# Optimization experiments

Hardware: AMD Instinct MI355X
Metric: run time of the kernel (lower is better)

The kernel has to match this reference:

```python
import jax, jax.numpy as jnp
import numpy as np

HIDDEN = 96
N_NODES = 50000
N_EDGES = 800000
IN_DIM = 256


def setup_inputs() -> dict:
    key = jax.random.key(0)
    ks = jax.random.split(key, 8)
    x = jax.random.normal(ks[0], (N_NODES, IN_DIM), dtype=jnp.float32)
    d = jax.random.uniform(ks[1], (N_NODES,), dtype=jnp.float32)
    src = jax.random.randint(ks[2], (N_EDGES,), 0, N_NODES, dtype=jnp.int32)
    dst = jax.random.randint(ks[3], (N_EDGES,), 0, N_NODES, dtype=jnp.int32)
    # Xavier-normal-ish init scaled like the torch module (gain 1.414)
    W_in = jax.random.normal(ks[4], (HIDDEN, IN_DIM), dtype=jnp.float32) * (1.414 * np.sqrt(2.0 / (HIDDEN + IN_DIM)))
    b_in = jnp.zeros((HIDDEN,), dtype=jnp.float32)
    W_gate = jax.random.normal(ks[5], (HIDDEN, 2 * HIDDEN), dtype=jnp.float32) * (1.414 * np.sqrt(2.0 / (3 * HIDDEN)))
    b_gate = jnp.zeros((HIDDEN,), dtype=jnp.float32)
    W_clf = jax.random.normal(ks[6], (2, HIDDEN), dtype=jnp.float32) * np.sqrt(2.0 / (2 + HIDDEN))
    b_clf = jnp.zeros((2,), dtype=jnp.float32)
    return {"x": x, "d": d, "src": src, "dst": dst,
            "W_in": W_in, "b_in": b_in, "W_gate": W_gate, "b_gate": b_gate,
            "W_clf": W_clf, "b_clf": b_clf}


def reference(x, d, src, dst, W_in, b_in, W_gate, b_gate, W_clf, b_clf):
    # h = input_gate(x)
    h = x @ W_in.T + b_in                                  # [N, H]
    # NOTE: the original loop reassigns the same h every iteration, so every
    # num_layer iteration produces identical (z, a); one pass is the exact math.
    h_src = h[src]                                         # [E, H] gather
    h_dst = h[dst]                                         # [E, H] gather
    h2 = jnp.concatenate([h_dst, h_src], axis=1)           # [E, 2H]
    a = jnp.tanh((h2 @ W_gate.T + b_gate) / np.sqrt(2.0 * HIDDEN))  # [E, H]
    e = d[dst] * d[src]                                    # [E]
    msg = h_src * a * e[:, None]                           # [E, H]
    z = jax.ops.segment_sum(msg, dst, num_segments=N_NODES)  # scatter-sum to dst
    z = jax.nn.log_softmax(z @ W_clf.T + b_clf, axis=-1)   # [N, 2]
    return (z, a)
```

## Files before the change

### kernel.cpp

```cpp
#include <hip/hip_runtime.h>
#include <math.h>

#define HIDDEN 96
#define NNODES 50000
#define NEDGES 800000
#define INDIM  256
#define RS 0.07216878364870323f

__global__ void repack_kernel(const float* __restrict__ Wg, const float* __restrict__ bg,
                              float* __restrict__ V, float* __restrict__ bias2) {
    int idx = blockIdx.x * 256 + threadIdx.x;
    if (idx < 192 * 96) {
        int j = idx / 96, k = idx % 96;
        float v = (j < 96) ? Wg[j * 192 + k] : Wg[(j - 96) * 192 + 96 + k];
        V[idx] = v * RS;
    }
    if (idx < 192) bias2[idx] = (idx < 96) ? bg[idx] * RS : 0.0f;
}

__global__ __launch_bounds__(256) void gemm_nt_bias(
    const float* __restrict__ A, const float* __restrict__ B,
    const float* __restrict__ bias, float* __restrict__ C,
    int M, int K, int ldc) {
    __shared__ float As[128][36];
    __shared__ float Bs[96][36];
    const int tid = threadIdx.x;
    const int m0 = blockIdx.x * 128;
    const int n0 = blockIdx.y * 96;
    const int te = tid >> 4;
    const int tc = tid & 15;
    const int ra = tid >> 3;
    const int ka = (tid & 7) * 4;

    float acc[8][6];
#pragma unroll
    for (int i = 0; i < 8; i++)
#pragma unroll
        for (int j = 0; j < 6; j++) acc[i][j] = 0.0f;

    for (int k0 = 0; k0 < K; k0 += 32) {
#pragma unroll
        for (int r = 0; r < 4; r++) {
            int row = m0 + ra + r * 32;
            float4 v = make_float4(0, 0, 0, 0);
            if (row < M) v = *(const float4*)&A[(size_t)row * K + k0 + ka];
            *(float4*)&As[ra + r * 32][ka] = v;
        }
#pragma unroll
        for (int r = 0; r < 3; r++) {
            int row = n0 + ra + r * 32;
            float4 v = *(const float4*)&B[(size_t)row * K + k0 + ka];
            *(float4*)&Bs[ra + r * 32][ka] = v;
        }
        __syncthreads();
#pragma unroll
        for (int k4 = 0; k4 < 32; k4 += 4) {
            float4 af[8], bf[6];
#pragma unroll
            for (int i = 0; i < 8; i++) af[i] = *(float4*)&As[8 * te + i][k4];
#pragma unroll
            for (int j = 0; j < 6; j++) bf[j] = *(float4*)&Bs[6 * tc + j][k4];
#pragma unroll
            for (int i = 0; i < 8; i++)
#pragma unroll
                for (int j = 0; j < 6; j++)
                    acc[i][j] += af[i].x * bf[j].x + af[i].y * bf[j].y +
                                 af[i].z * bf[j].z + af[i].w * bf[j].w;
        }
        __syncthreads();
    }
#pragma unroll
    for (int i = 0; i < 8; i++) {
        int row = m0 + 8 * te + i;
        if (row < M) {
#pragma unroll
            for (int j = 0; j < 6; j++) {
                int col = n0 + 6 * tc + j;
                C[(size_t)row * ldc + col] = acc[i][j] + bias[col];
            }
        }
    }
}

__global__ void hist_kernel(const int* __restrict__ dst, int* __restrict__ counts) {
    int i = blockIdx.x * 256 + threadIdx.x;
    if (i < NEDGES) atomicAdd(&counts[dst[i]], 1);
}

__global__ __launch_bounds__(512) void scan1_kernel(const int* __restrict__ counts,
                                                    int* __restrict__ offsets,
                                                    int* __restrict__ btot) {
    __shared__ int sh[512];
    int tid = threadIdx.x;
    int i = blockIdx.x * 512 + tid;
    int v = (i < NNODES) ? counts[i] : 0;
    sh[tid] = v;
    __syncthreads();
    for (int off = 1; off < 512; off <<= 1) {
        int tmp = 0;
        if (tid >= off) tmp = sh[tid - off];
        __syncthreads();
        if (tid >= off) sh[tid] += tmp;
        __syncthreads();
    }
    if (i < NNODES) offsets[i] = sh[tid] - v;
    if (tid == 511) btot[blockIdx.x] = sh[511];
}

__global__ __launch_bounds__(128) void scan2_kernel(int* __restrict__ btot, int nb) {
    __shared__ int sh[128];
    int tid = threadIdx.x;
    int v = (tid < nb) ? btot[tid] : 0;
    sh[tid] = v;
    __syncthreads();
    for (int off = 1; off < 128; off <<= 1) {
        int tmp = 0;
        if (tid >= off) tmp = sh[tid - off];
        __syncthreads();
        if (tid >= off) sh[tid] += tmp;
        __syncthreads();
    }
    if (tid < nb) btot[tid] = sh[tid] - v;
}

__global__ __launch_bounds__(512) void scan3_kernel(int* __restrict__ offsets,
                                                    const int* __restrict__ btot) {
    int i = blockIdx.x * 512 + threadIdx.x;
    if (i < NNODES) offsets[i] += btot[blockIdx.x];
    if (i == 0) offsets[NNODES] = NEDGES;
}

__global__ void scatter_kernel(const int* __restrict__ src, const int* __restrict__ dst,
                               const int* __restrict__ offsets, int* __restrict__ cursor,
                               int* __restrict__ eidx, int* __restrict__ esrc) {
    int e = blockIdx.x * 256 + threadIdx.x;
    if (e < NEDGES) {
        int t = dst[e];
        int pos = offsets[t] + atomicAdd(&cursor[t], 1);
        eidx[pos] = e;
        esrc[pos] = src[e];
    }
}

#define GPB 32
#define TPG 24
__global__ __launch_bounds__(768) void agg_kernel(
    const float* __restrict__ P, const float* __restrict__ h,
    const float* __restrict__ dvec, const int* __restrict__ offsets,
    const int* __restrict__ eidx, const int* __restrict__ esrc,
    const float* __restrict__ Wc, const float* __restrict__ bc,
    float* __restrict__ a_out, float* __restrict__ z_out) {
    __shared__ float red0[GPB * TPG];
    __shared__ float red1[GPB * TPG];
    const int t = threadIdx.x;
    const int g = t / TPG;
    const int c = t % TPG;
    const int node = blockIdx.x * GPB + g;
    float s0 = 0.0f, s1 = 0.0f;
    if (node < NNODES) {
        float4 pd = *(const float4*)&P[(size_t)node * 192 + 4 * c];
        float dt = dvec[node];
        int start = offsets[node], end = offsets[node + 1];
        float4 z4 = make_float4(0, 0, 0, 0);
        for (int i = start; i < end; i++) {
            int e = eidx[i];
            int s = esrc[i];
            float4 ps = *(const float4*)&P[(size_t)s * 192 + 96 + 4 * c];
            float4 hs = *(const float4*)&h[(size_t)s * 96 + 4 * c];
            float ee = dt * dvec[s];
            float4 a4;
            a4.x = tanhf(pd.x + ps.x);
            a4.y = tanhf(pd.y + ps.y);
            a4.z = tanhf(pd.z + ps.z);
            a4.w = tanhf(pd.w + ps.w);
            *(float4*)&a_out[(size_t)e * 96 + 4 * c] = a4;
            z4.x += hs.x * a4.x * ee;
            z4.y += hs.y * a4.y * ee;
            z4.z += hs.z * a4.z * ee;
            z4.w += hs.w * a4.w * ee;
        }
        float4 w0 = *(const float4*)&Wc[4 * c];
        float4 w1 = *(const float4*)&Wc[96 + 4 * c];
        s0 = z4.x * w0.x + z4.y * w0.y + z4.z * w0.z + z4.w * w0.w;
        s1 = z4.x * w1.x + z4.y * w1.y + z4.z * w1.z + z4.w * w1.w;
    }
    red0[t] = s0;
    red1[t] = s1;
    __syncthreads();
    if (c == 0 && node < NNODES) {
        float a0 = bc[0], a1 = bc[1];
#pragma unroll
        for (int k = 0; k < TPG; k++) { a0 += red0[t + k]; a1 += red1[t + k]; }
        float m = fmaxf(a0, a1);
        float lse = m + logf(expf(a0 - m) + expf(a1 - m));
        z_out[2 * node + 0] = a0 - lse;
        z_out[2 * node + 1] = a1 - lse;
    }
}

extern "C" void kernel_launch(void* const* d_in, const int* in_sizes, int n_in,
                              void* d_out, int out_size, void* d_ws, size_t ws_size,
                              hipStream_t stream) {
    const float* x    = (const float*)d_in[0];
    const float* dvec = (const float*)d_in[1];
    const int*   src  = (const int*)d_in[2];
    const int*   dst  = (const int*)d_in[3];
    const float* W_in = (const float*)d_in[4];
    const float* b_in = (const float*)d_in[5];
    const float* W_g  = (const float*)d_in[6];
    const float* b_g  = (const float*)d_in[7];
    const float* W_c  = (const float*)d_in[8];
    const float* b_c  = (const float*)d_in[9];

    float* z_out = (float*)d_out;
    float* a_out = (float*)d_out + 2 * NNODES;

    char* ws = (char*)d_ws;
    float* h       = (float*)(ws);
    float* P       = (float*)(ws + 19200000);
    float* V       = (float*)(ws + 57600000);
    float* b2      = (float*)(ws + 57673728);
    int*   offsets = (int*)  (ws + 57674752);
    int*   counts  = (int*)  (ws + 57874816);
    int*   cursor  = (int*)  (ws + 58074880);
    int*   btot    = (int*)  (ws + 58274944);
    int*   eidx    = (int*)  (ws + 58275456);
    int*   esrc    = (int*)  (ws + 61475456);

    hipMemsetAsync(counts, 0, NNODES * sizeof(int), stream);
    hipMemsetAsync(cursor, 0, NNODES * sizeof(int), stream);

    repack_kernel<<<dim3((192 * 96 + 255) / 256), 256, 0, stream>>>(W_g, b_g, V, b2);
    gemm_nt_bias<<<dim3((NNODES + 127) / 128, 1), 256, 0, stream>>>(x, W_in, b_in, h, NNODES, INDIM, HIDDEN);
    gemm_nt_bias<<<dim3((NNODES + 127) / 128, 2), 256, 0, stream>>>(h, V, b2, P, NNODES, HIDDEN, 192);

    const int NB = (NNODES + 511) / 512;
    hist_kernel<<<dim3((NEDGES + 255) / 256), 256, 0, stream>>>(dst, counts);
    scan1_kernel<<<dim3(NB), 512, 0, stream>>>(counts, offsets, btot);
    scan2_kernel<<<dim3(1), 128, 0, stream>>>(btot, NB);
    scan3_kernel<<<dim3(NB), 512, 0, stream>>>(offsets, btot);
    scatter_kernel<<<dim3((NEDGES + 255) / 256), 256, 0, stream>>>(src, dst, offsets, cursor, eidx, esrc);

    agg_kernel<<<dim3((NNODES + GPB - 1) / GPB), GPB * TPG, 0, stream>>>(
        P, h, dvec, offsets, eidx, esrc, W_c, b_c, a_out, z_out);
}
```

Measured before the change: 738.9 us.

## Interleave source projection with h, pack edge pairs, use fast tanh and nontemporal stores

The first GEMM now writes h into the upper half of a 192-wide row buffer. A new dual GEMM writes the dst projection to a separate array and the src projection into the lower half of that same row, so each gathered source row yields both the projection and h from one contiguous 768-byte region. Edge index and source are packed into an int2 array so one load replaces two. The aggregation loop also uses an exp2/rcp tanh approximation and nontemporal stores for the large a output, cutting transcendental cost and cache pollution at a small accuracy risk.

```diff
diff --git a/kernel.cpp b/kernel.cpp
--- a/kernel.cpp
+++ b/kernel.cpp
@@ -6,6 +6,14 @@
 #define NEDGES 800000
 #define INDIM  256
 #define RS 0.07216878364870323f
+
+typedef float f32x4 __attribute__((ext_vector_type(4)));
+
+__device__ __forceinline__ float fast_tanh(float x) {
+    float e = __builtin_amdgcn_exp2f(fabsf(x) * 2.8853900817779268f);
+    float t = 1.0f - 2.0f * __builtin_amdgcn_rcpf(1.0f + e);
+    return copysignf(t, x);
+}
 
 __global__ void repack_kernel(const float* __restrict__ Wg, const float* __restrict__ bg,
                               float* __restrict__ V, float* __restrict__ bias2) {
@@ -19,14 +27,14 @@
 }
 
 __global__ __launch_bounds__(256) void gemm_nt_bias(
-    const float* __restrict__ A, const float* __restrict__ B,
+    const float* __restrict__ A, int lda,
+    const float* __restrict__ B,
     const float* __restrict__ bias, float* __restrict__ C,
     int M, int K, int ldc) {
     __shared__ float As[128][36];
     __shared__ float Bs[96][36];
     const int tid = threadIdx.x;
     const int m0 = blockIdx.x * 128;
-    const int n0 = blockIdx.y * 96;
     const int te = tid >> 4;
     const int tc = tid & 15;
     const int ra = tid >> 3;
@@ -43,14 +51,14 @@
         for (int r = 0; r < 4; r++) {
             int row = m0 + ra + r * 32;
             float4 v = make_float4(0, 0, 0, 0);
-            if (row < M) v = *(const float4*)&A[(size_t)row * K + k0 + ka];
+            if (row < M) v = *(const float4*)&A[(size_t)row * lda + k0 + ka];
             *(float4*)&As[ra + r * 32][ka] = v;
         }
 #pragma unroll
         for (int r = 0; r < 3; r++) {
-            int row = n0 + ra + r * 32;
+            int row = ra + r * 32;
             float4 v = *(const float4*)&B[(size_t)row * K + k0 + ka];
-            *(float4*)&Bs[ra + r * 32][ka] = v;
+            *(float4*)&Bs[row][ka] = v;
         }
         __syncthreads();
 #pragma unroll
@@ -75,8 +83,78 @@
         if (row < M) {
 #pragma unroll
             for (int j = 0; j < 6; j++) {
-                int col = n0 + 6 * tc + j;
+                int col = 6 * tc + j;
                 C[(size_t)row * ldc + col] = acc[i][j] + bias[col];
+            }
+        }
+    }
+}
+
+__global__ __launch_bounds__(256) void gemm2_dual(
+    const float* __restrict__ Ah,
+    const float* __restrict__ V,
+    const float* __restrict__ b2,
+    float* __restrict__ Dm,
+    float* __restrict__ SH,
+    int M) {
+    __shared__ float As[128][36];
+    __shared__ float Bs[96][36];
+    const int tid = threadIdx.x;
+    const int m0 = blockIdx.x * 128;
+    const int half = blockIdx.y;
+    const int n0 = half * 96;
+    const int te = tid >> 4;
+    const int tc = tid & 15;
+    const int ra = tid >> 3;
+    const int ka = (tid & 7) * 4;
+
+    float acc[8][6];
+#pragma unroll
+    for (int i = 0; i < 8; i++)
+#pragma unroll
+        for (int j = 0; j < 6; j++) acc[i][j] = 0.0f;
+
+    for (int k0 = 0; k0 < 96; k0 += 32) {
+#pragma unroll
+        for (int r = 0; r < 4; r++) {
+            int row = m0 + ra + r * 32;
+            float4 v = make_float4(0, 0, 0, 0);
+            if (row < M) v = *(const float4*)&Ah[(size_t)row * 192 + k0 + ka];
+            *(float4*)&As[ra + r * 32][ka] = v;
+        }
+#pragma unroll
+        for (int r = 0; r < 3; r++) {
+            int row = ra + r * 32;
+            float4 v = *(const float4*)&V[(size_t)(n0 + row) * 96 + k0 + ka];
+            *(float4*)&Bs[row][ka] = v;
+        }
+        __syncthreads();
+#pragma unroll
+        for (int k4 = 0; k4 < 32; k4 += 4) {
+            float4 af[8], bf[6];
+#pragma unroll
+            for (int i = 0; i < 8; i++) af[i] = *(float4*)&As[8 * te + i][k4];
+#pragma unroll
+            for (int j = 0; j < 6; j++) bf[j] = *(float4*)&Bs[6 * tc + j][k4];
+#pragma unroll
+            for (int i = 0; i < 8; i++)
+#pragma unroll
+                for (int j = 0; j < 6; j++)
+                    acc[i][j] += af[i].x * bf[j].x + af[i].y * bf[j].y +
+                                 af[i].z * bf[j].z + af[i].w * bf[j].w;
+        }
+        __syncthreads();
+    }
+    float* Cp = half ? SH : Dm;
+    const int ldc = half ? 192 : 96;
+#pragma unroll
+    for (int i = 0; i < 8; i++) {
+        int row = m0 + 8 * te + i;
+        if (row < M) {
+#pragma unroll
+            for (int j = 0; j < 6; j++) {
+                int col = 6 * tc + j;
+                Cp[(size_t)row * ldc + col] = acc[i][j] + b2[n0 + col];
             }
         }
     }
@@ -132,22 +210,21 @@
 
 __global__ void scatter_kernel(const int* __restrict__ src, const int* __restrict__ dst,
                                const int* __restrict__ offsets, int* __restrict__ cursor,
-                               int* __restrict__ eidx, int* __restrict__ esrc) {
+                               int2* __restrict__ epair) {
     int e = blockIdx.x * 256 + threadIdx.x;
     if (e < NEDGES) {
         int t = dst[e];
         int pos = offsets[t] + atomicAdd(&cursor[t], 1);
-        eidx[pos] = e;
-        esrc[pos] = src[e];
+        epair[pos] = make_int2(e, src[e]);
     }
 }
 
 #define GPB 32
 #define TPG 24
 __global__ __launch_bounds__(768) void agg_kernel(
-    const float* __restrict__ P, const float* __restrict__ h,
+    const float* __restrict__ Dm, const float* __restrict__ SH,
     const float* __restrict__ dvec, const int* __restrict__ offsets,
-    const int* __restrict__ eidx, const int* __restrict__ esrc,
+    const int2* __restrict__ epair,
     const float* __restrict__ Wc, const float* __restrict__ bc,
     float* __restrict__ a_out, float* __restrict__ z_out) {
     __shared__ float red0[GPB * TPG];
@@ -158,22 +235,22 @@
     const int node = blockIdx.x * GPB + g;
     float s0 = 0.0f, s1 = 0.0f;
     if (node < NNODES) {
-        float4 pd = *(const float4*)&P[(size_t)node * 192 + 4 * c];
+        float4 pd = *(const float4*)&Dm[(size_t)node * 96 + 4 * c];
         float dt = dvec[node];
         int start = offsets[node], end = offsets[node + 1];
         float4 z4 = make_float4(0, 0, 0, 0);
         for (int i = start; i < end; i++) {
-            int e = eidx[i];
-            int s = esrc[i];
-            float4 ps = *(const float4*)&P[(size_t)s * 192 + 96 + 4 * c];
-            float4 hs = *(const float4*)&h[(size_t)s * 96 + 4 * c];
-            float ee = dt * dvec[s];
-            float4 a4;
-            a4.x = tanhf(pd.x + ps.x);
-            a4.y = tanhf(pd.y + ps.y);
-            a4.z = tanhf(pd.z + ps.z);
-            a4.w = tanhf(pd.w + ps.w);
-            *(float4*)&a_out[(size_t)e * 96 + 4 * c] = a4;
+            int2 ep = epair[i];
+            const float* base = &SH[(size_t)ep.y * 192];
+            float4 ps = *(const float4*)(base + 4 * c);
+            float4 hs = *(const float4*)(base + 96 + 4 * c);
+            float ee = dt * dvec[ep.y];
+            f32x4 a4;
+            a4.x = fast_tanh(pd.x + ps.x);
+            a4.y = fast_tanh(pd.y + ps.y);
+            a4.z = fast_tanh(pd.z + ps.z);
+            a4.w = fast_tanh(pd.w + ps.w);
+            __builtin_nontemporal_store(a4, (f32x4*)&a_out[(size_t)ep.x * 96 + 4 * c]);
             z4.x += hs.x * a4.x * ee;
             z4.y += hs.y * a4.y * ee;
             z4.z += hs.z * a4.z * ee;
@@ -216,31 +293,32 @@
     float* a_out = (float*)d_out + 2 * NNODES;
 
     char* ws = (char*)d_ws;
-    float* h       = (float*)(ws);
-    float* P       = (float*)(ws + 19200000);
+    float* SH      = (float*)(ws);
+    float* Dm      = (float*)(ws + 38400000);
     float* V       = (float*)(ws + 57600000);
     float* b2      = (float*)(ws + 57673728);
     int*   offsets = (int*)  (ws + 57674752);
     int*   counts  = (int*)  (ws + 57874816);
     int*   cursor  = (int*)  (ws + 58074880);
     int*   btot    = (int*)  (ws + 58274944);
-    int*   eidx    = (int*)  (ws + 58275456);
-    int*   esrc    = (int*)  (ws + 61475456);
+    int2*  epair   = (int2*) (ws + 58275456);
 
     hipMemsetAsync(counts, 0, NNODES * sizeof(int), stream);
     hipMemsetAsync(cursor, 0, NNODES * sizeof(int), stream);
 
     repack_kernel<<<dim3((192 * 96 + 255) / 256), 256, 0, stream>>>(W_g, b_g, V, b2);
-    gemm_nt_bias<<<dim3((NNODES + 127) / 128, 1), 256, 0, stream>>>(x, W_in, b_in, h, NNODES, INDIM, HIDDEN);
-    gemm_nt_bias<<<dim3((NNODES + 127) / 128, 2), 256, 0, stream>>>(h, V, b2, P, NNODES, HIDDEN, 192);
+    gemm_nt_bias<<<dim3((NNODES + 127) / 128), 256, 0, stream>>>(
+        x, INDIM, W_in, b_in, SH + 96, NNODES, INDIM, 192);
+    gemm2_dual<<<dim3((NNODES + 127) / 128, 2), 256, 0, stream>>>(
+        SH + 96, V, b2, Dm, SH, NNODES);
 
     const int NB = (NNODES + 511) / 512;
     hist_kernel<<<dim3((NEDGES + 255) / 256), 256, 0, stream>>>(dst, counts);
     scan1_kernel<<<dim3(NB), 512, 0, stream>>>(counts, offsets, btot);
     scan2_kernel<<<dim3(1), 128, 0, stream>>>(btot, NB);
     scan3_kernel<<<dim3(NB), 512, 0, stream>>>(offsets, btot);
-    scatter_kernel<<<dim3((NEDGES + 255) / 256), 256, 0, stream>>>(src, dst, offsets, cursor, eidx, esrc);
+    scatter_kernel<<<dim3((NEDGES + 255) / 256), 256, 0, stream>>>(src, dst, offsets, cursor, epair);
 
     agg_kernel<<<dim3((NNODES + GPB - 1) / GPB), GPB * TPG, 0, stream>>>(
-        P, h, dvec, offsets, eidx, esrc, W_c, b_c, a_out, z_out);
-}
+        Dm, SH, dvec, offsets, epair, W_c, b_c, a_out, z_out);
+}
```

New measurement: 767.5 us. +3.9%, slower.
